# Kernel tuning notes

Measured on AMD Instinct MI355X. Metric: run time of the kernel, lower is better.

Reference implementation:

```python
import jax, jax.numpy as jnp
import numpy as np

N, E, D, L = 50000, 800000, 128, 4


def setup_inputs() -> dict:
    key = jax.random.key(0)
    k0, k1, k2, k3 = jax.random.split(key, 4)
    x = jax.random.normal(k0, (N, D), dtype=jnp.float32)
    edge_index = jax.random.randint(k1, (2, E), 0, N, dtype=jnp.int32)
    # per-layer GCNConv weights [L, D, D] and biases [L, D]
    W = jax.random.normal(k2, (L, D, D), dtype=jnp.float32) * (1.0 / np.sqrt(D))
    b = jax.random.normal(k3, (L, D), dtype=jnp.float32) * 0.01
    batch_index = jnp.zeros((N,), dtype=jnp.int32)
    node_rankings = jnp.zeros((N,), dtype=jnp.int32)
    return {"x": x, "edge_index": edge_index, "batch_index": batch_index,
            "node_rankings": node_rankings, "W": W, "b": b}


def reference(x, edge_index, batch_index, node_rankings, W, b):
    # NullControl contributes 0; dropout_rate=0 / eval -> identity.
    n = x.shape[0]
    loops = jnp.arange(n, dtype=edge_index.dtype)
    row = jnp.concatenate([edge_index[0], loops])  # sources (with self-loops)
    col = jnp.concatenate([edge_index[1], loops])  # destinations
    # symmetric GCN normalization: deg over destinations, norm = d_i^-1/2 d_j^-1/2
    deg = jax.ops.segment_sum(jnp.ones_like(row, dtype=x.dtype), col, num_segments=n)
    dinv = jnp.where(deg > 0, jax.lax.rsqrt(deg), 0.0)
    norm = dinv[row] * dinv[col]  # [E+N]
    for l in range(W.shape[0]):
        h = x @ W[l]                      # [N, D] dense transform
        msg = h[row] * norm[:, None]      # [E+N, D] gathered, scaled messages
        agg = jax.ops.segment_sum(msg, col, num_segments=n)  # scatter-add
        x = jax.nn.relu(agg + b[l])       # control(=0) + bias + relu
    return x
```

## Files before the change

### kernel.cpp

```cpp
#include <hip/hip_runtime.h>

#define D 128
#define NLAYERS 4

typedef unsigned short ushort_t;
typedef unsigned int uint_t;

__device__ __forceinline__ ushort_t f2bf(float f) {
    uint_t u = __float_as_uint(f);
    u += 0x7FFFu + ((u >> 16) & 1u);
    return (ushort_t)(u >> 16);
}
__device__ __forceinline__ float bf_lo(uint_t u) {
    return __uint_as_float(u << 16);
}
__device__ __forceinline__ float bf_hi(uint_t u) {
    return __uint_as_float(u & 0xFFFF0000u);
}


__global__ void k_count_deg(const int* __restrict__ dsts, int E,
                            int* __restrict__ deg, int* __restrict__ slot) {
    int i = blockIdx.x * blockDim.x + threadIdx.x;
    if (i < E) slot[i] = atomicAdd(&deg[dsts[i]], 1);
}

__global__ void k_dinv(const int* __restrict__ deg, int n, float* __restrict__ dinv) {
    int i = blockIdx.x * blockDim.x + threadIdx.x;
    if (i < n) dinv[i] = rsqrtf((float)(deg[i] + 1));
}

__global__ void k_scan1(const int* __restrict__ deg, int n, int* __restrict__ out,
                        int* __restrict__ partials) {
    __shared__ int wsum[4];
    int tid = threadIdx.x;
    int base = blockIdx.x * 1024 + tid * 4;
    int d0 = (base + 0 < n) ? deg[base + 0] : 0;
    int d1 = (base + 1 < n) ? deg[base + 1] : 0;
    int d2 = (base + 2 < n) ? deg[base + 2] : 0;
    int d3 = (base + 3 < n) ? deg[base + 3] : 0;
    int s = d0 + d1 + d2 + d3;
    int lane = tid & 63;
    int incl = s;
    #pragma unroll
    for (int off = 1; off < 64; off <<= 1) {
        int y = __shfl_up(incl, off);
        if (lane >= off) incl += y;
    }
    int wid = tid >> 6;
    if (lane == 63) wsum[wid] = incl;
    __syncthreads();
    int wprev = 0;
    for (int w = 0; w < wid; w++) wprev += wsum[w];
    int excl = wprev + (incl - s);
    if (base + 0 < n) out[base + 0] = excl;
    if (base + 1 < n) out[base + 1] = excl + d0;
    if (base + 2 < n) out[base + 2] = excl + d0 + d1;
    if (base + 3 < n) out[base + 3] = excl + d0 + d1 + d2;
    if (tid == 255) partials[blockIdx.x] = wprev + incl;
}

__global__ void k_scan2(int* partials, int nb) {
    if (threadIdx.x == 0 && blockIdx.x == 0) {
        int acc = 0;
        for (int i = 0; i < nb; i++) { int t = partials[i]; partials[i] = acc; acc += t; }
    }
}

__global__ void k_scan3(int* __restrict__ row_ptr, const int* __restrict__ partials,
                        int n, int E) {
    int i = blockIdx.x * blockDim.x + threadIdx.x;
    if (i < n) row_ptr[i] += partials[i >> 10];
    if (i == 0) row_ptr[n] = E;
}

__global__ void k_place(const int* __restrict__ srcs, const int* __restrict__ dsts, int E,
                        const int* __restrict__ row_ptr, const int* __restrict__ slot,
                        const float* __restrict__ dinv, int2* __restrict__ ew) {
    int i = blockIdx.x * blockDim.x + threadIdx.x;
    if (i >= E) return;
    int c = dsts[i], r = srcs[i];
    int pos = row_ptr[c] + slot[i];
    int2 v;
    v.x = r;
    v.y = __float_as_int(dinv[r]);
    ew[pos] = v;
}

__global__ void k_tobf16(const float* __restrict__ x, ushort_t* __restrict__ xh,
                         int total4) {
    int i = blockIdx.x * blockDim.x + threadIdx.x;
    if (i >= total4) return;
    float4 v = ((const float4*)x)[i];
    ushort_t r0 = f2bf(v.x), r1 = f2bf(v.y), r2 = f2bf(v.z), r3 = f2bf(v.w);
    uint2 o;
    o.x = (uint_t)r0 | ((uint_t)r1 << 16);
    o.y = (uint_t)r2 | ((uint_t)r3 << 16);
    ((uint2*)xh)[i] = o;
}

__global__ __launch_bounds__(256) void k_aggregate(
    const ushort_t* __restrict__ xh, const int* __restrict__ row_ptr,
    const int2* __restrict__ ew, const float* __restrict__ dinv,
    float* __restrict__ s, int n) {
    int gwave = (blockIdx.x * 256 + threadIdx.x) >> 6;
    if (gwave >= n) return;
    int lane = threadIdx.x & 63;
    int node = gwave;
    float di = dinv[node];
    uint_t su = *(const uint_t*)(xh + (size_t)node * D + 2 * lane);
    float acc0 = di * bf_lo(su);
    float acc1 = di * bf_hi(su);
    int e = row_ptr[node];
    int end = row_ptr[node + 1];
    for (; e + 4 <= end; e += 4) {
        int2 e0 = ew[e];
        int2 e1 = ew[e + 1];
        int2 e2 = ew[e + 2];
        int2 e3 = ew[e + 3];
        uint_t u0 = *(const uint_t*)(xh + (size_t)e0.x * D + 2 * lane);
        uint_t u1 = *(const uint_t*)(xh + (size_t)e1.x * D + 2 * lane);
        uint_t u2 = *(const uint_t*)(xh + (size_t)e2.x * D + 2 * lane);
        uint_t u3 = *(const uint_t*)(xh + (size_t)e3.x * D + 2 * lane);
        float w0 = __int_as_float(e0.y), w1 = __int_as_float(e1.y);
        float w2 = __int_as_float(e2.y), w3 = __int_as_float(e3.y);
        acc0 += w0 * bf_lo(u0) + w1 * bf_lo(u1) + w2 * bf_lo(u2) + w3 * bf_lo(u3);
        acc1 += w0 * bf_hi(u0) + w1 * bf_hi(u1) + w2 * bf_hi(u2) + w3 * bf_hi(u3);
    }
    for (; e < end; ++e) {
        int2 e0 = ew[e];
        uint_t u0 = *(const uint_t*)(xh + (size_t)e0.x * D + 2 * lane);
        float w0 = __int_as_float(e0.y);
        acc0 += w0 * bf_lo(u0);
        acc1 += w0 * bf_hi(u0);
    }
    float2 o;
    o.x = di * acc0;
    o.y = di * acc1;
    ((float2*)(s + (size_t)node * D))[lane] = o;
}

__global__ __launch_bounds__(256) void k_gemm_bias_relu(
    const float* __restrict__ A, const float* __restrict__ Wl,
    const float* __restrict__ bias, float* __restrict__ out_f32,
    ushort_t* __restrict__ out_bf, int n) {
    __shared__ float As[64][D];
    int tid = threadIdx.x;
    int brow = blockIdx.x * 64;
    #pragma unroll
    for (int p = 0; p < 8; p++) {
        int r = p * 8 + (tid >> 5);
        int c = (tid & 31) * 4;
        int gr = brow + r;
        if (gr > n - 1) gr = n - 1;
        float4 v = *(const float4*)(A + (size_t)gr * D + c);
        *(float4*)&As[r][c] = v;
    }
    __syncthreads();
    int rg = tid >> 5;
    int cg = tid & 31;
    int c0 = cg * 4;
    float acc[8][4];
    #pragma unroll
    for (int j = 0; j < 8; j++)
        #pragma unroll
        for (int q = 0; q < 4; q++) acc[j][q] = 0.f;

    for (int k0 = 0; k0 < D; k0 += 4) {
        float4 w0 = *(const float4*)(Wl + (size_t)(k0 + 0) * D + c0);
        float4 w1 = *(const float4*)(Wl + (size_t)(k0 + 1) * D + c0);
        float4 w2 = *(const float4*)(Wl + (size_t)(k0 + 2) * D + c0);
        float4 w3 = *(const float4*)(Wl + (size_t)(k0 + 3) * D + c0);
        #pragma unroll
        for (int j = 0; j < 8; j++) {
            float4 a = *(const float4*)&As[rg * 8 + j][k0];
            acc[j][0] += a.x * w0.x + a.y * w1.x + a.z * w2.x + a.w * w3.x;
            acc[j][1] += a.x * w0.y + a.y * w1.y + a.z * w2.y + a.w * w3.y;
            acc[j][2] += a.x * w0.z + a.y * w1.z + a.z * w2.z + a.w * w3.z;
            acc[j][3] += a.x * w0.w + a.y * w1.w + a.z * w2.w + a.w * w3.w;
        }
    }
    float4 bv = *(const float4*)(bias + c0);
    #pragma unroll
    for (int j = 0; j < 8; j++) {
        int gr = brow + rg * 8 + j;
        if (gr < n) {
            float o0 = fmaxf(acc[j][0] + bv.x, 0.f);
            float o1 = fmaxf(acc[j][1] + bv.y, 0.f);
            float o2 = fmaxf(acc[j][2] + bv.z, 0.f);
            float o3 = fmaxf(acc[j][3] + bv.w, 0.f);
            if (out_bf) {
                uint2 o;
                o.x = (uint_t)f2bf(o0) | ((uint_t)f2bf(o1) << 16);
                o.y = (uint_t)f2bf(o2) | ((uint_t)f2bf(o3) << 16);
                *(uint2*)(out_bf + (size_t)gr * D + c0) = o;
            } else {
                float4 o;
                o.x = o0; o.y = o1; o.z = o2; o.w = o3;
                *(float4*)(out_f32 + (size_t)gr * D + c0) = o;
            }
        }
    }
}


extern "C" void kernel_launch(void* const* d_in, const int* in_sizes, int n_in,
                              void* d_out, int out_size, void* d_ws, size_t ws_size,
                              hipStream_t stream) {
    const float* x   = (const float*)d_in[0];
    const int* eidx  = (const int*)d_in[1];
    const float* W   = (const float*)d_in[4];
    const float* b   = (const float*)d_in[5];
    float* out       = (float*)d_out;

    const int N = in_sizes[0] / D;
    const int E = in_sizes[1] / 2;
    const int* srcs = eidx;
    const int* dsts = eidx + E;

    char* ws = (char*)d_ws;
    size_t off = 0;
    auto alloc = [&](size_t bytes) -> void* {
        void* p = ws + off;
        off = (off + bytes + 511) & ~(size_t)511;
        return p;
    };
    int*      deg      = (int*)alloc((size_t)N * 4);
    float*    dinv     = (float*)alloc((size_t)N * 4);
    int*      row_ptr  = (int*)alloc((size_t)(N + 1) * 4);
    int*      partials = (int*)alloc(256 * 4);
    int2*     ew       = (int2*)alloc((size_t)E * 8);
    float*    s_buf    = (float*)alloc((size_t)N * D * 4);
    ushort_t* xh0      = (ushort_t*)alloc((size_t)N * D * 2);
    ushort_t* xh1      = (ushort_t*)alloc((size_t)N * D * 2);
    int*      slot     = (int*)s_buf;
    (void)ws_size; (void)n_in; (void)out_size;

    hipMemsetAsync(deg, 0, (size_t)N * 4, stream);

    int tE = (E + 255) / 256;
    int tN = (N + 255) / 256;
    int nbScan = (N + 1023) / 1024;

    k_count_deg<<<tE, 256, 0, stream>>>(dsts, E, deg, slot);
    k_dinv<<<tN, 256, 0, stream>>>(deg, N, dinv);
    k_scan1<<<nbScan, 256, 0, stream>>>(deg, N, row_ptr, partials);
    k_scan2<<<1, 64, 0, stream>>>(partials, nbScan);
    k_scan3<<<tN, 256, 0, stream>>>(row_ptr, partials, N, E);
    k_place<<<tE, 256, 0, stream>>>(srcs, dsts, E, row_ptr, slot, dinv, ew);

    int total4 = N * D / 4;
    k_tobf16<<<(total4 + 255) / 256, 256, 0, stream>>>(x, xh0, total4);

    int aggBlocks = (N + 3) / 4;
    int gemmBlocks = (N + 63) / 64;

    const ushort_t* xin = xh0;
    for (int l = 0; l < NLAYERS; l++) {
        k_aggregate<<<aggBlocks, 256, 0, stream>>>(xin, row_ptr, ew, dinv, s_buf, N);
        bool last = (l == NLAYERS - 1);
        ushort_t* xout = last ? nullptr : ((l & 1) ? xh0 : xh1);
        k_gemm_bias_relu<<<gemmBlocks, 256, 0, stream>>>(
            s_buf, W + (size_t)l * D * D, b + (size_t)l * D,
            last ? out : nullptr, xout, N);
        xin = xout;
    }
}
```

Measured before the change: 443.3 us.

## Split wavefront into four edge groups with 16-byte gathers, fuse dinv into scan

The aggregation kernel now splits each 64-lane wavefront into four 16-lane subgroups. Each subgroup gathers a different edge's full 256-byte bf16 row with uint4 loads, and the partial sums are combined with cross-lane shuffles at the end. This cuts the per-edge instruction count and keeps more independent memory requests in flight. The cost is extra shuffle reductions, idle lanes during the tail loop, and only a quarter of lanes doing the final store. Separately, the dinv computation is folded into the first scan kernel to drop one launch.

```diff
diff --git a/kernel.cpp b/kernel.cpp
--- a/kernel.cpp
+++ b/kernel.cpp
@@ -25,13 +25,8 @@
     if (i < E) slot[i] = atomicAdd(&deg[dsts[i]], 1);
 }
 
-__global__ void k_dinv(const int* __restrict__ deg, int n, float* __restrict__ dinv) {
-    int i = blockIdx.x * blockDim.x + threadIdx.x;
-    if (i < n) dinv[i] = rsqrtf((float)(deg[i] + 1));
-}
-
 __global__ void k_scan1(const int* __restrict__ deg, int n, int* __restrict__ out,
-                        int* __restrict__ partials) {
+                        int* __restrict__ partials, float* __restrict__ dinv) {
     __shared__ int wsum[4];
     int tid = threadIdx.x;
     int base = blockIdx.x * 1024 + tid * 4;
@@ -39,6 +34,10 @@
     int d1 = (base + 1 < n) ? deg[base + 1] : 0;
     int d2 = (base + 2 < n) ? deg[base + 2] : 0;
     int d3 = (base + 3 < n) ? deg[base + 3] : 0;
+    if (base + 0 < n) dinv[base + 0] = rsqrtf((float)(d0 + 1));
+    if (base + 1 < n) dinv[base + 1] = rsqrtf((float)(d1 + 1));
+    if (base + 2 < n) dinv[base + 2] = rsqrtf((float)(d2 + 1));
+    if (base + 3 < n) dinv[base + 3] = rsqrtf((float)(d3 + 1));
     int s = d0 + d1 + d2 + d3;
     int lane = tid & 63;
     int incl = s;
@@ -92,10 +91,9 @@
     int i = blockIdx.x * blockDim.x + threadIdx.x;
     if (i >= total4) return;
     float4 v = ((const float4*)x)[i];
-    ushort_t r0 = f2bf(v.x), r1 = f2bf(v.y), r2 = f2bf(v.z), r3 = f2bf(v.w);
     uint2 o;
-    o.x = (uint_t)r0 | ((uint_t)r1 << 16);
-    o.y = (uint_t)r2 | ((uint_t)r3 << 16);
+    o.x = (uint_t)f2bf(v.x) | ((uint_t)f2bf(v.y) << 16);
+    o.y = (uint_t)f2bf(v.z) | ((uint_t)f2bf(v.w) << 16);
     ((uint2*)xh)[i] = o;
 }
 
@@ -106,38 +104,61 @@
     int gwave = (blockIdx.x * 256 + threadIdx.x) >> 6;
     if (gwave >= n) return;
     int lane = threadIdx.x & 63;
+    int sub = lane >> 4;
+    int t = lane & 15;
     int node = gwave;
     float di = dinv[node];
-    uint_t su = *(const uint_t*)(xh + (size_t)node * D + 2 * lane);
-    float acc0 = di * bf_lo(su);
-    float acc1 = di * bf_hi(su);
-    int e = row_ptr[node];
-    int end = row_ptr[node + 1];
-    for (; e + 4 <= end; e += 4) {
-        int2 e0 = ew[e];
-        int2 e1 = ew[e + 1];
-        int2 e2 = ew[e + 2];
-        int2 e3 = ew[e + 3];
-        uint_t u0 = *(const uint_t*)(xh + (size_t)e0.x * D + 2 * lane);
-        uint_t u1 = *(const uint_t*)(xh + (size_t)e1.x * D + 2 * lane);
-        uint_t u2 = *(const uint_t*)(xh + (size_t)e2.x * D + 2 * lane);
-        uint_t u3 = *(const uint_t*)(xh + (size_t)e3.x * D + 2 * lane);
-        float w0 = __int_as_float(e0.y), w1 = __int_as_float(e1.y);
-        float w2 = __int_as_float(e2.y), w3 = __int_as_float(e3.y);
-        acc0 += w0 * bf_lo(u0) + w1 * bf_lo(u1) + w2 * bf_lo(u2) + w3 * bf_lo(u3);
-        acc1 += w0 * bf_hi(u0) + w1 * bf_hi(u1) + w2 * bf_hi(u2) + w3 * bf_hi(u3);
-    }
-    for (; e < end; ++e) {
-        int2 e0 = ew[e];
-        uint_t u0 = *(const uint_t*)(xh + (size_t)e0.x * D + 2 * lane);
-        float w0 = __int_as_float(e0.y);
-        acc0 += w0 * bf_lo(u0);
-        acc1 += w0 * bf_hi(u0);
-    }
-    float2 o;
-    o.x = di * acc0;
-    o.y = di * acc1;
-    ((float2*)(s + (size_t)node * D))[lane] = o;
+
+    float acc[8];
+    {
+        uint4 v = *(const uint4*)(xh + (size_t)node * D + t * 8);
+        float w = (sub == 0) ? di : 0.f;
+        acc[0] = w * bf_lo(v.x); acc[1] = w * bf_hi(v.x);
+        acc[2] = w * bf_lo(v.y); acc[3] = w * bf_hi(v.y);
+        acc[4] = w * bf_lo(v.z); acc[5] = w * bf_hi(v.z);
+        acc[6] = w * bf_lo(v.w); acc[7] = w * bf_hi(v.w);
+    }
+    int e = row_ptr[node], end = row_ptr[node + 1];
+    for (; e + 8 <= end; e += 8) {
+        int2 g0 = ew[e + sub];
+        int2 g1 = ew[e + 4 + sub];
+        uint4 v0 = *(const uint4*)(xh + (size_t)g0.x * D + t * 8);
+        uint4 v1 = *(const uint4*)(xh + (size_t)g1.x * D + t * 8);
+        float w0 = __int_as_float(g0.y);
+        float w1 = __int_as_float(g1.y);
+        acc[0] += w0 * bf_lo(v0.x); acc[1] += w0 * bf_hi(v0.x);
+        acc[2] += w0 * bf_lo(v0.y); acc[3] += w0 * bf_hi(v0.y);
+        acc[4] += w0 * bf_lo(v0.z); acc[5] += w0 * bf_hi(v0.z);
+        acc[6] += w0 * bf_lo(v0.w); acc[7] += w0 * bf_hi(v0.w);
+        acc[0] += w1 * bf_lo(v1.x); acc[1] += w1 * bf_hi(v1.x);
+        acc[2] += w1 * bf_lo(v1.y); acc[3] += w1 * bf_hi(v1.y);
+        acc[4] += w1 * bf_lo(v1.z); acc[5] += w1 * bf_hi(v1.z);
+        acc[6] += w1 * bf_lo(v1.w); acc[7] += w1 * bf_hi(v1.w);
+    }
+    for (; e < end; e += 4) {
+        int rem = end - e;
+        int k = (sub < rem) ? sub : 0;
+        int2 g = ew[e + k];
+        float w = (sub < rem) ? __int_as_float(g.y) : 0.f;
+        uint4 v = *(const uint4*)(xh + (size_t)g.x * D + t * 8);
+        acc[0] += w * bf_lo(v.x); acc[1] += w * bf_hi(v.x);
+        acc[2] += w * bf_lo(v.y); acc[3] += w * bf_hi(v.y);
+        acc[4] += w * bf_lo(v.z); acc[5] += w * bf_hi(v.z);
+        acc[6] += w * bf_lo(v.w); acc[7] += w * bf_hi(v.w);
+    }
+    #pragma unroll
+    for (int q = 0; q < 8; q++) {
+        acc[q] += __shfl_xor(acc[q], 16);
+        acc[q] += __shfl_xor(acc[q], 32);
+    }
+    if (sub == 0) {
+        float* dst = s + (size_t)node * D + t * 8;
+        float4 o0, o1;
+        o0.x = di * acc[0]; o0.y = di * acc[1]; o0.z = di * acc[2]; o0.w = di * acc[3];
+        o1.x = di * acc[4]; o1.y = di * acc[5]; o1.z = di * acc[6]; o1.w = di * acc[7];
+        *(float4*)dst = o0;
+        *(float4*)(dst + 4) = o1;
+    }
 }
 
 __global__ __launch_bounds__(256) void k_gemm_bias_relu(
@@ -243,8 +264,7 @@
     int nbScan = (N + 1023) / 1024;
 
     k_count_deg<<<tE, 256, 0, stream>>>(dsts, E, deg, slot);
-    k_dinv<<<tN, 256, 0, stream>>>(deg, N, dinv);
-    k_scan1<<<nbScan, 256, 0, stream>>>(deg, N, row_ptr, partials);
+    k_scan1<<<nbScan, 256, 0, stream>>>(deg, N, row_ptr, partials, dinv);
     k_scan2<<<1, 64, 0, stream>>>(partials, nbScan);
     k_scan3<<<tN, 256, 0, stream>>>(row_ptr, partials, N, E);
     k_place<<<tE, 256, 0, stream>>>(srcs, dsts, E, row_ptr, slot, dinv, ew);
```

Measured after the change: 416.1 us. -6.1%, faster.
